# Kernel tuning notes

Hardware: AMD Instinct MI355X
Metric: run time of the kernel (lower is better)

Reference implementation:

```python
import jax, jax.numpy as jnp
import numpy as np

DIM = 1024
N_HEADS = 16
HEAD_DIM = DIM // N_HEADS


def setup_inputs() -> dict:
    key = jax.random.key(0)
    ks = jax.random.split(key, 5)
    scale = 1.0 / np.sqrt(DIM)
    x = jax.random.normal(ks[0], (2, 2048, DIM), dtype=jnp.float32)
    W_qkv = jax.random.normal(ks[1], (DIM, 3 * DIM), dtype=jnp.float32) * scale
    b_qkv = jax.random.normal(ks[2], (3 * DIM,), dtype=jnp.float32) * 0.01
    W_proj = jax.random.normal(ks[3], (DIM, DIM), dtype=jnp.float32) * scale
    b_proj = jax.random.normal(ks[4], (DIM,), dtype=jnp.float32) * 0.01
    return {"x": x, "W_qkv": W_qkv, "b_qkv": b_qkv, "W_proj": W_proj, "b_proj": b_proj}


def reference(x, W_qkv, b_qkv, W_proj, b_proj):
    B, T, C = x.shape
    qkv = x @ W_qkv + b_qkv  # [B,T,3C]
    q, k, v = jnp.split(qkv, 3, axis=2)
    # [B,T,C] -> [B,H,T,Dh]
    def heads(y):
        return y.reshape(B, T, N_HEADS, HEAD_DIM).transpose(0, 2, 1, 3)
    q, k, v = heads(q), heads(k), heads(v)
    inv_sqrt_dh = 1.0 / jnp.sqrt(jnp.asarray(HEAD_DIM, dtype=x.dtype))
    attn = jnp.einsum('bhqd,bhkd->bhqk', q, k) * inv_sqrt_dh
    attn = jax.nn.softmax(attn, axis=-1)
    out = jnp.einsum('bhqk,bhkd->bhqd', attn, v)
    out = out.transpose(0, 2, 1, 3).reshape(B, T, C)
    return out @ W_proj + b_proj
```

## Files before the change

kernel.cpp:

```cpp
#include <hip/hip_runtime.h>
#include <hip/hip_bf16.h>
#include <math.h>

using bf16 = __hip_bfloat16;

typedef __bf16 bf16x8 __attribute__((ext_vector_type(8)));
typedef __bf16 bf16x4 __attribute__((ext_vector_type(4)));
typedef float  f32x4  __attribute__((ext_vector_type(4)));
typedef float  f32x16 __attribute__((ext_vector_type(16)));

constexpr int Bb = 2;
constexpr int Ts = 2048;
constexpr int Cc = 1024;
constexpr int Hh = 16;
constexpr int Dh = 64;
constexpr int Mm = Bb * Ts;
constexpr int Nqkv = 3 * Cc;
constexpr int BHTD = Bb * Hh * Ts * Dh;

__device__ __forceinline__
void gll16(const __bf16* g, __bf16* l)
{
    __builtin_amdgcn_global_load_lds(
        (const __attribute__((address_space(1))) unsigned int*)g,
        (__attribute__((address_space(3))) unsigned int*)l,
        16, 0, 0);
}

__global__ __launch_bounds__(256)
void prep_all(const float* __restrict__ x, __bf16* __restrict__ Xb,
              const float* __restrict__ Wq, __bf16* __restrict__ Wqt,
              const float* __restrict__ Wp, __bf16* __restrict__ Wpt)
{
    __shared__ __bf16 tl[64][72];
    const int bid = blockIdx.x;
    const int t = threadIdx.x;

    if (bid < 4096) {
        int i = (bid * 256 + t) * 4;
        float4 v = *(const float4*)(x + i);
        bf16x4 o = { (__bf16)v.x, (__bf16)v.y, (__bf16)v.z, (__bf16)v.w };
        *(bf16x4*)(Xb + i) = o;
        return;
    }
    const float* W; __bf16* Wt; int cols, bx, by;
    if (bid < 4096 + 768) {
        W = Wq; Wt = Wqt; cols = Nqkv;
        bx = (bid - 4096) % 48; by = (bid - 4096) / 48;
    } else {
        W = Wp; Wt = Wpt; cols = Cc;
        bx = (bid - 4864) % 16; by = (bid - 4864) / 16;
    }
    const int c0 = bx * 64;
    const int r0 = by * 64;
    #pragma unroll
    for (int i = 0; i < 4; i++) {
        int e = t + 256 * i;
        int r = e >> 4, c4 = (e & 15) * 4;
        float4 v = *(const float4*)(W + (r0 + r) * cols + c0 + c4);
        bf16x4 o = { (__bf16)v.x, (__bf16)v.y, (__bf16)v.z, (__bf16)v.w };
        *(bf16x4*)&tl[r][c4] = o;
    }
    __syncthreads();
    #pragma unroll
    for (int i = 0; i < 4; i++) {
        int e = t + 256 * i;
        int n = e >> 4, k4 = (e & 15) * 4;
        bf16x4 o = { tl[k4][n], tl[k4 + 1][n], tl[k4 + 2][n], tl[k4 + 3][n] };
        *(bf16x4*)(Wt + (c0 + n) * 1024 + r0 + k4) = o;
    }
}

template<int BM>
__device__ __forceinline__
void gemm_core_tb(__bf16* sbuf,
                  const __bf16* __restrict__ A, const __bf16* __restrict__ Bt,
                  int m0, int n0, int wm, int wn, int quad, int l16, int t,
                  f32x4 (&acc)[4][4])
{
    constexpr int MT   = BM / 32;
    constexpr int AG   = BM / 64;
    constexpr int STEP = (BM + 128) * 32;

    const int wave = t >> 6;
    const int lane = t & 63;
    const int srow = lane >> 2;
    const int scol = ((lane & 3) ^ (srow & 3)) * 8;

    const __bf16* Ag = A  + (size_t)(m0 + wave * (BM / 4) + srow) * 1024 + scol;
    const __bf16* Bg = Bt + (size_t)(n0 + wave * 32 + srow) * 1024 + scol;

    {
        __bf16* Alp = sbuf;
        __bf16* Blp = sbuf + BM * 32;
        #pragma unroll
        for (int g = 0; g < AG; g++)
            gll16(Ag + (size_t)g * 16 * 1024, &Alp[(wave * (BM / 4) + g * 16) * 32]);
        gll16(Bg,                      &Blp[(wave * 32) * 32]);
        gll16(Bg + (size_t)16 * 1024,  &Blp[(wave * 32 + 16) * 32]);
    }

    const int cb = (quad ^ (l16 & 3)) * 16;

    for (int j = 0; j < 32; j++) {
        const int p = j % 3;
        if (j < 31) {
            const int pn = (j + 1) % 3;
            const int k1 = (j + 1) * 32;
            __bf16* Alp = sbuf + pn * STEP;
            __bf16* Blp = Alp + BM * 32;
            #pragma unroll
            for (int g = 0; g < AG; g++)
                gll16(Ag + k1 + (size_t)g * 16 * 1024,
                      &Alp[(wave * (BM / 4) + g * 16) * 32]);
            gll16(Bg + k1,                     &Blp[(wave * 32) * 32]);
            gll16(Bg + k1 + (size_t)16 * 1024, &Blp[(wave * 32 + 16) * 32]);
            if constexpr (AG == 2) asm volatile("s_waitcnt vmcnt(4)" ::: "memory");
            else                   asm volatile("s_waitcnt vmcnt(3)" ::: "memory");
        } else {
            asm volatile("s_waitcnt vmcnt(0)" ::: "memory");
        }
        __builtin_amdgcn_s_barrier();
        __builtin_amdgcn_sched_barrier(0);

        const char* Alp = (const char*)(sbuf + p * STEP);
        const char* Blp = (const char*)(sbuf + p * STEP + BM * 32);
        bf16x8 af[MT], bfr[4];
        #pragma unroll
        for (int mt = 0; mt < MT; mt++)
            af[mt] = *(const bf16x8*)(Alp + (wm * (BM / 2) + mt * 16 + l16) * 64 + cb);
        #pragma unroll
        for (int nt = 0; nt < 4; nt++)
            bfr[nt] = *(const bf16x8*)(Blp + (wn * 64 + nt * 16 + l16) * 64 + cb);
        #pragma unroll
        for (int mt = 0; mt < MT; mt++)
            #pragma unroll
            for (int nt = 0; nt < 4; nt++)
                acc[mt][nt] = __builtin_amdgcn_mfma_f32_16x16x32_bf16(
                    af[mt], bfr[nt], acc[mt][nt], 0, 0, 0);
    }
    __syncthreads();
}

__global__ __launch_bounds__(512, 2)
void qkv_mfma(const __bf16* __restrict__ A, const __bf16* __restrict__ Bt,
              const float* __restrict__ bias, __bf16* __restrict__ qkv)
{
    __shared__ __align__(16) __bf16 smem[2 * 512 * 64];
    typedef __bf16 (*ebuf_p)[64][72];
    ebuf_p ebuf = (ebuf_p)smem;

    const int t    = threadIdx.x;
    const int wave = t >> 6;
    const int lane = t & 63;
    const int quad = lane >> 4;
    const int l16  = lane & 15;
    const int wm   = wave >> 2;
    const int wn   = wave & 3;
    const int bid  = blockIdx.x;
    const int swb  = (bid & 7) * 24 + (bid >> 3);
    const int n0 = (swb % 12) * 256;
    const int m0 = (swb / 12) * 256;

    f32x4 acc[8][4];
    #pragma unroll
    for (int i = 0; i < 8; i++)
        #pragma unroll
        for (int j = 0; j < 4; j++)
            acc[i][j] = f32x4{0.f, 0.f, 0.f, 0.f};

    const int srow = lane >> 3;
    const int scol = ((lane & 7) ^ srow) * 8;
    const __bf16* Ag = A  + (size_t)(m0 + wave * 32 + srow) * 1024 + scol;
    const __bf16* Bg = Bt + (size_t)(n0 + wave * 32 + srow) * 1024 + scol;

    {
        __bf16* Alp = smem;
        __bf16* Blp = smem + 256 * 64;
        #pragma unroll
        for (int g = 0; g < 4; g++) {
            gll16(Ag + (size_t)g * 8 * 1024, &Alp[(wave * 32 + g * 8) * 64]);
            gll16(Bg + (size_t)g * 8 * 1024, &Blp[(wave * 32 + g * 8) * 64]);
        }
    }

    for (int j = 0; j < 16; j++) {
        const int p = j & 1;
        asm volatile("s_waitcnt vmcnt(0)" ::: "memory");
        __builtin_amdgcn_s_barrier();
        __builtin_amdgcn_sched_barrier(0);
        if (j < 15) {
            const int k1 = (j + 1) * 64;
            __bf16* Alp = smem + (p ^ 1) * (512 * 64);
            __bf16* Blp = Alp + 256 * 64;
            #pragma unroll
            for (int g = 0; g < 4; g++) {
                gll16(Ag + k1 + (size_t)g * 8 * 1024, &Alp[(wave * 32 + g * 8) * 64]);
                gll16(Bg + k1 + (size_t)g * 8 * 1024, &Blp[(wave * 32 + g * 8) * 64]);
            }
        }
        const char* Alp = (const char*)(smem + p * (512 * 64));
        const char* Blp = Alp + 256 * 64 * 2;

        #pragma unroll
        for (int kk = 0; kk < 2; kk++) {
            const int cb = ((kk * 4 + quad) ^ (l16 & 7)) * 16;
            bf16x8 af[8], bfr[4];
            #pragma unroll
            for (int mt = 0; mt < 8; mt++)
                af[mt] = *(const bf16x8*)(Alp + (wm * 128 + mt * 16 + l16) * 128 + cb);
            #pragma unroll
            for (int nt = 0; nt < 4; nt++)
                bfr[nt] = *(const bf16x8*)(Blp + (wn * 64 + nt * 16 + l16) * 128 + cb);
            __builtin_amdgcn_s_setprio(1);
            #pragma unroll
            for (int mt = 0; mt < 8; mt++)
                #pragma unroll
                for (int nt = 0; nt < 4; nt++)
                    acc[mt][nt] = __builtin_amdgcn_mfma_f32_16x16x32_bf16(
                        af[mt], bfr[nt], acc[mt][nt], 0, 0, 0);
            __builtin_amdgcn_s_setprio(0);
        }
    }
    __syncthreads();

    const int nw0 = n0 + wn * 64;
    const int which = nw0 >> 10;
    const int h = (nw0 & 1023) >> 6;

    #pragma unroll
    for (int hh = 0; hh < 2; hh++) {
        if (which == 2) {
            #pragma unroll
            for (int nt = 0; nt < 4; nt++) {
                float bs = bias[nw0 + nt * 16 + l16];
                #pragma unroll
                for (int ml = 0; ml < 4; ml++) {
                    const int mt = hh * 4 + ml;
                    #pragma unroll
                    for (int r = 0; r < 4; r++)
                        ebuf[wave][nt * 16 + l16][ml * 16 + quad * 4 + r] =
                            (__bf16)(acc[mt][nt][r] + bs);
                }
            }
            const int mbase = m0 + wm * 128 + hh * 64;
            const int b   = mbase >> 11;
            const int tt0 = mbase & 2047;
            __bf16* vb0 = &qkv[2 * (size_t)BHTD +
                               ((size_t)(b * 16 + h) * 64) * 2048 + tt0];
            const int q4 = (lane & 3) * 16;
            #pragma unroll
            for (int p2 = 0; p2 < 4; p2++) {
                const int d = 16 * p2 + (lane >> 2);
                const __bf16* src = &ebuf[wave][d][q4];
                __bf16* drow = vb0 + (size_t)d * 2048 + q4;
                *(bf16x8*)drow       = *(const bf16x8*)src;
                *(bf16x8*)(drow + 8) = *(const bf16x8*)(src + 8);
            }
        } else {
            #pragma unroll
            for (int nt = 0; nt < 4; nt++) {
                float bs = bias[nw0 + nt * 16 + l16];
                #pragma unroll
                for (int ml = 0; ml < 4; ml++) {
                    const int mt = hh * 4 + ml;
                    #pragma unroll
                    for (int r = 0; r < 4; r++)
                        ebuf[wave][ml * 16 + quad * 4 + r][nt * 16 + l16] =
                            (__bf16)(acc[mt][nt][r] + bs);
                }
            }
            int m = m0 + wm * 128 + hh * 64 + lane;
            int b = m >> 11;
            int tt = m & 2047;
            __bf16* dst = &qkv[which * (size_t)BHTD +
                               (((size_t)(b * 16 + h) * 2048 + tt) * 64)];
            #pragma unroll
            for (int c = 0; c < 8; c++)
                *(bf16x8*)(dst + c * 8) = *(const bf16x8*)&ebuf[wave][lane][c * 8];
        }
    }
}

__global__ __launch_bounds__(256)
void proj_mfma(const __bf16* __restrict__ A, const __bf16* __restrict__ Bt,
               const float* __restrict__ bias, float* __restrict__ out)
{
    __shared__ __align__(16) __bf16 smem[3 * (64 + 128) * 32];

    const int t    = threadIdx.x;
    const int wave = t >> 6;
    const int lane = t & 63;
    const int quad = lane >> 4;
    const int l16  = lane & 15;
    const int wm   = wave >> 1, wn = wave & 1;
    const int bid  = blockIdx.x;
    const int n0 = (bid & 7) * 128;
    const int m0 = (bid >> 3) * 64;

    f32x4 acc[4][4];
    #pragma unroll
    for (int i = 0; i < 4; i++)
        #pragma unroll
        for (int j = 0; j < 4; j++)
            acc[i][j] = f32x4{0.f, 0.f, 0.f, 0.f};

    gemm_core_tb<64>(smem, A, Bt, m0, n0, wm, wn, quad, l16, t, acc);

    #pragma unroll
    for (int nt = 0; nt < 4; nt++) {
        int n = n0 + wn * 64 + nt * 16 + l16;
        float bs = bias[n];
        #pragma unroll
        for (int mt = 0; mt < 2; mt++) {
            #pragma unroll
            for (int r = 0; r < 4; r++) {
                int m = m0 + wm * 32 + mt * 16 + quad * 4 + r;
                out[m * 1024 + n] = acc[mt][nt][r] + bs;
            }
        }
    }
}

__global__ __launch_bounds__(512, 2)
void attn_mfma(const __bf16* __restrict__ Q, const __bf16* __restrict__ K,
               const __bf16* __restrict__ VT, __bf16* __restrict__ O)
{
    __shared__ __bf16 sK[2][3][64 * 64];
    __shared__ __bf16 sV[2][3][64 * 64];
    __shared__ float  slsum[4][2][64];

    const int t    = threadIdx.x;
    const int wave = t >> 6;
    const int lane = t & 63;
    const int qg   = wave & 3;
    const int kh   = wave >> 2;
    const int c    = lane & 31;
    const int hi   = lane >> 5;
    const int hx   = hi * 16;
    const int sw   = (c & 7) << 4;

    const int blk = blockIdx.x;
    const int bh  = blk & 31;
    const int qc  = blk >> 5;
    const int q0  = qc * 256 + qg * 64;

    const __bf16* Qp = Q  + ((size_t)bh * Ts + q0) * Dh;
    const __bf16* Kp = K  + (size_t)bh * Ts * Dh;
    const __bf16* Vp = VT + (size_t)bh * Dh * Ts;

    const float qscale = 0.125f * 1.44269504088896f;
    bf16x8 qf[2][4];
    #pragma unroll
    for (int qs = 0; qs < 2; qs++)
        #pragma unroll
        for (int ds = 0; ds < 4; ds++) {
            bf16x8 v = *(const bf16x8*)(Qp + (qs * 32 + c) * Dh + ds * 16 + hi * 8);
            #pragma unroll
            for (int i = 0; i < 8; i++) v[i] = (__bf16)(qscale * (float)v[i]);
            qf[qs][ds] = v;
        }

    f32x16 accO[2][2];
    #pragma unroll
    for (int qs = 0; qs < 2; qs++)
        #pragma unroll
        for (int dt = 0; dt < 2; dt++)
            #pragma unroll
            for (int i = 0; i < 16; i++) accO[qs][dt][i] = 0.f;
    float lsum[2] = {0.f, 0.f};

    const f32x16 z16 = {0.f, 0.f, 0.f, 0.f, 0.f, 0.f, 0.f, 0.f,
                        0.f, 0.f, 0.f, 0.f, 0.f, 0.f, 0.f, 0.f};

    const int r0 = qg * 8 + (lane >> 3);
    const int s8 = ((lane & 7) ^ (r0 & 7)) * 8;
    const __bf16* kg0 = Kp + (size_t)(kh * 1024 + r0) * Dh + s8;
    const __bf16* kg1 = kg0 + 32 * Dh;
    const __bf16* vg0 = Vp + (size_t)r0 * Ts + kh * 1024 + s8;
    const __bf16* vg1 = vg0 + (size_t)32 * Ts;

    gll16(kg0, &sK[kh][0][qg * 512]);
    gll16(kg1, &sK[kh][0][2048 + qg * 512]);
    gll16(vg0, &sV[kh][0][qg * 512]);
    gll16(vg1, &sV[kh][0][2048 + qg * 512]);

    for (int j = 0; j < 16; j++) {
        const int p = j % 3;
        if (j < 15) {
            const int pn = (j + 1) % 3;
            gll16(kg0 + (j + 1) * 4096, &sK[kh][pn][qg * 512]);
            gll16(kg1 + (j + 1) * 4096, &sK[kh][pn][2048 + qg * 512]);
            gll16(vg0 + (j + 1) * 64,   &sV[kh][pn][qg * 512]);
            gll16(vg1 + (j + 1) * 64,   &sV[kh][pn][2048 + qg * 512]);
            asm volatile("s_waitcnt vmcnt(4)" ::: "memory");
        } else {
            asm volatile("s_waitcnt vmcnt(0)" ::: "memory");
        }
        __builtin_amdgcn_s_barrier();
        __builtin_amdgcn_sched_barrier(0);

        const char* kb = (const char*)&sK[kh][p][0];
        const char* vb = (const char*)&sV[kh][p][0];

        bf16x8 kf[2][4];
        #pragma unroll
        for (int kt = 0; kt < 2; kt++) {
            const char* rbase = kb + (kt * 32 + c) * 128;
            #pragma unroll
            for (int ds = 0; ds < 4; ds++)
                kf[kt][ds] = *(const bf16x8*)(rbase + ((ds * 32 + hx) ^ sw));
        }

        f32x16 st[2][2];
        __builtin_amdgcn_s_setprio(1);
        #pragma unroll
        for (int kt = 0; kt < 2; kt++)
            #pragma unroll
            for (int qs = 0; qs < 2; qs++)
                st[qs][kt] = __builtin_amdgcn_mfma_f32_32x32x16_bf16(
                    kf[kt][0], qf[qs][0], z16, 0, 0, 0);
        #pragma unroll
        for (int ds = 1; ds < 4; ds++)
            #pragma unroll
            for (int kt = 0; kt < 2; kt++)
                #pragma unroll
                for (int qs = 0; qs < 2; qs++)
                    st[qs][kt] = __builtin_amdgcn_mfma_f32_32x32x16_bf16(
                        kf[kt][ds], qf[qs][ds], st[qs][kt], 0, 0, 0);
        __builtin_amdgcn_s_setprio(0);

        bf16x8 pa[2][4];
        #pragma unroll
        for (int qs = 0; qs < 2; qs++) {
            unsigned pk[2][8];
            #pragma unroll
            for (int kt = 0; kt < 2; kt++) {
                float sum0 = 0.f, sum1 = 0.f;
                #pragma unroll
                for (int r = 0; r < 16; r++) {
                    float pv = __builtin_amdgcn_exp2f(st[qs][kt][r]);
                    st[qs][kt][r] = pv;
                    if (r & 1) sum1 += pv; else sum0 += pv;
                }
                lsum[qs] += sum0 + sum1;
                #pragma unroll
                for (int r2 = 0; r2 < 8; r2++) {
                    unsigned d;
                    asm("v_cvt_pk_bf16_f32 %0, %1, %2"
                        : "=v"(d)
                        : "v"(st[qs][kt][2 * r2]), "v"(st[qs][kt][2 * r2 + 1]));
                    pk[kt][r2] = d;
                }
            }
            #pragma unroll
            for (int s = 0; s < 4; s++) {
                const int kt = s >> 1, r4 = (s & 1) * 4;
                unsigned x0 = pk[kt][r4 + 0], y0 = pk[kt][r4 + 2];
                unsigned x1 = pk[kt][r4 + 1], y1 = pk[kt][r4 + 3];
                asm("v_permlane32_swap_b32 %0, %1" : "+v"(x0), "+v"(y0));
                asm("v_permlane32_swap_b32 %0, %1" : "+v"(x1), "+v"(y1));
                union { unsigned u[4]; bf16x8 b; } pu;
                pu.u[0] = x0; pu.u[1] = x1; pu.u[2] = y0; pu.u[3] = y1;
                pa[qs][s] = pu.b;
            }
        }

        __builtin_amdgcn_s_setprio(1);
        #pragma unroll
        for (int s = 0; s < 4; s++)
            #pragma unroll
            for (int dt = 0; dt < 2; dt++) {
                bf16x8 vf = *(const bf16x8*)(vb + (dt * 32 + c) * 128 +
                                             ((s * 32 + hx) ^ sw));
                #pragma unroll
                for (int qs = 0; qs < 2; qs++)
                    accO[qs][dt] = __builtin_amdgcn_mfma_f32_32x32x16_bf16(
                        pa[qs][s], vf, accO[qs][dt], 0, 0, 0);
            }
        __builtin_amdgcn_s_setprio(0);
    }

    __syncthreads();

    float* pb = (qg < 2) ? (float*)&sK[0][0][0] + qg * 4096
                         : (float*)&sV[0][0][0] + (qg - 2) * 4096;
    if (kh == 1) {
        #pragma unroll
        for (int qs = 0; qs < 2; qs++) {
            #pragma unroll
            for (int dt = 0; dt < 2; dt++)
                #pragma unroll
                for (int r = 0; r < 16; r++)
                    pb[((qs * 2 + dt) << 10) + (r << 6) + lane] = accO[qs][dt][r];
            slsum[qg][qs][lane] = lsum[qs];
        }
    }
    __syncthreads();
    if (kh == 0) {
        #pragma unroll
        for (int qs = 0; qs < 2; qs++) {
            #pragma unroll
            for (int dt = 0; dt < 2; dt++)
                #pragma unroll
                for (int r = 0; r < 16; r++)
                    accO[qs][dt][r] += pb[((qs * 2 + dt) << 10) + (r << 6) + lane];
            lsum[qs] += slsum[qg][qs][lane];
        }

        const int b = bh >> 4, h = bh & 15;
        #pragma unroll
        for (int qs = 0; qs < 2; qs++) {
            float l = lsum[qs] + __shfl_xor(lsum[qs], 32);
            float linv = 1.f / l;
            #pragma unroll
            for (int r = 0; r < 16; r++) {
                const int qrow = (r & 3) + 8 * (r >> 2) + 4 * hi;
                float inv = __shfl(linv, qrow);
                __bf16* Op = O + ((size_t)(b * Ts + q0 + qs * 32 + qrow)) * Cc +
                             h * 64 + c;
                Op[0]  = (__bf16)(accO[qs][0][r] * inv);
                Op[32] = (__bf16)(accO[qs][1][r] * inv);
            }
        }
    }
}

extern "C" void kernel_launch(void* const* d_in, const int* in_sizes, int n_in,
                              void* d_out, int out_size, void* d_ws, size_t ws_size,
                              hipStream_t stream)
{
    (void)in_sizes; (void)n_in; (void)out_size; (void)ws_size;
    const float* x     = (const float*)d_in[0];
    const float* Wqkv  = (const float*)d_in[1];
    const float* bqkv  = (const float*)d_in[2];
    const float* Wproj = (const float*)d_in[3];
    const float* bproj = (const float*)d_in[4];
    float* out = (float*)d_out;

    __bf16* ws   = (__bf16*)d_ws;
    __bf16* Qw   = ws;
    __bf16* XbAO = ws + 3 * (size_t)BHTD;
    __bf16* Wqt  = XbAO + (size_t)Mm * Cc;
    __bf16* Wpt  = Wqt + (size_t)Nqkv * Cc;

    prep_all<<<dim3(5120), 256, 0, stream>>>(x, XbAO, Wqkv, Wqt, Wproj, Wpt);
    qkv_mfma<<<dim3(192), 512, 0, stream>>>(XbAO, Wqt, bqkv, Qw);
    attn_mfma<<<dim3(256), 512, 0, stream>>>(
        Qw, Qw + BHTD, Qw + 2 * (size_t)BHTD, XbAO);
    proj_mfma<<<dim3(512), 256, 0, stream>>>(XbAO, Wpt, bproj, out);
}
```

Before: 177.8 us.

## Enlarge proj GEMM tile to 128x128 with BK=64 double buffering; coarsen x conversion

The projection GEMM moves from a 64x128 tile with a three-stage BK=32 pipeline to a 128x128 tile with double-buffered BK=64 loads, an 8-way XOR swizzle and MFMA priority hints. Its grid is halved to 256 blocks. The intent is more reuse per loaded tile and fewer barriers per unit of K. The x-to-bf16 conversion in prep_all now does four chunks per block, which cuts the block count and removes the now-unused shared gemm core. The costs are fewer blocks to fill the CUs in proj, which may underfill a 256-CU device, and a full vmcnt(0) wait each iteration that reduces load/compute overlap.

Result: no change. 177.2 us (-0.4%).

```diff
diff --git a/kernel.cpp b/kernel.cpp
--- a/kernel.cpp
+++ b/kernel.cpp
@@ -36,20 +36,23 @@
     const int bid = blockIdx.x;
     const int t = threadIdx.x;
 
-    if (bid < 4096) {
-        int i = (bid * 256 + t) * 4;
-        float4 v = *(const float4*)(x + i);
-        bf16x4 o = { (__bf16)v.x, (__bf16)v.y, (__bf16)v.z, (__bf16)v.w };
-        *(bf16x4*)(Xb + i) = o;
+    if (bid < 1024) {
+        #pragma unroll
+        for (int s = 0; s < 4; s++) {
+            int i = (bid * 256 + t + s * 262144) * 4;
+            float4 v = *(const float4*)(x + i);
+            bf16x4 o = { (__bf16)v.x, (__bf16)v.y, (__bf16)v.z, (__bf16)v.w };
+            *(bf16x4*)(Xb + i) = o;
+        }
         return;
     }
     const float* W; __bf16* Wt; int cols, bx, by;
-    if (bid < 4096 + 768) {
+    if (bid < 1024 + 768) {
         W = Wq; Wt = Wqt; cols = Nqkv;
-        bx = (bid - 4096) % 48; by = (bid - 4096) / 48;
+        bx = (bid - 1024) % 48; by = (bid - 1024) / 48;
     } else {
         W = Wp; Wt = Wpt; cols = Cc;
-        bx = (bid - 4864) % 16; by = (bid - 4864) / 16;
+        bx = (bid - 1792) % 16; by = (bid - 1792) / 16;
     }
     const int c0 = bx * 64;
     const int r0 = by * 64;
@@ -69,77 +72,6 @@
         bf16x4 o = { tl[k4][n], tl[k4 + 1][n], tl[k4 + 2][n], tl[k4 + 3][n] };
         *(bf16x4*)(Wt + (c0 + n) * 1024 + r0 + k4) = o;
     }
-}
-
-template<int BM>
-__device__ __forceinline__
-void gemm_core_tb(__bf16* sbuf,
-                  const __bf16* __restrict__ A, const __bf16* __restrict__ Bt,
-                  int m0, int n0, int wm, int wn, int quad, int l16, int t,
-                  f32x4 (&acc)[4][4])
-{
-    constexpr int MT   = BM / 32;
-    constexpr int AG   = BM / 64;
-    constexpr int STEP = (BM + 128) * 32;
-
-    const int wave = t >> 6;
-    const int lane = t & 63;
-    const int srow = lane >> 2;
-    const int scol = ((lane & 3) ^ (srow & 3)) * 8;
-
-    const __bf16* Ag = A  + (size_t)(m0 + wave * (BM / 4) + srow) * 1024 + scol;
-    const __bf16* Bg = Bt + (size_t)(n0 + wave * 32 + srow) * 1024 + scol;
-
-    {
-        __bf16* Alp = sbuf;
-        __bf16* Blp = sbuf + BM * 32;
-        #pragma unroll
-        for (int g = 0; g < AG; g++)
-            gll16(Ag + (size_t)g * 16 * 1024, &Alp[(wave * (BM / 4) + g * 16) * 32]);
-        gll16(Bg,                      &Blp[(wave * 32) * 32]);
-        gll16(Bg + (size_t)16 * 1024,  &Blp[(wave * 32 + 16) * 32]);
-    }
-
-    const int cb = (quad ^ (l16 & 3)) * 16;
-
-    for (int j = 0; j < 32; j++) {
-        const int p = j % 3;
-        if (j < 31) {
-            const int pn = (j + 1) % 3;
-            const int k1 = (j + 1) * 32;
-            __bf16* Alp = sbuf + pn * STEP;
-            __bf16* Blp = Alp + BM * 32;
-            #pragma unroll
-            for (int g = 0; g < AG; g++)
-                gll16(Ag + k1 + (size_t)g * 16 * 1024,
-                      &Alp[(wave * (BM / 4) + g * 16) * 32]);
-            gll16(Bg + k1,                     &Blp[(wave * 32) * 32]);
-            gll16(Bg + k1 + (size_t)16 * 1024, &Blp[(wave * 32 + 16) * 32]);
-            if constexpr (AG == 2) asm volatile("s_waitcnt vmcnt(4)" ::: "memory");
-            else                   asm volatile("s_waitcnt vmcnt(3)" ::: "memory");
-        } else {
-            asm volatile("s_waitcnt vmcnt(0)" ::: "memory");
-        }
-        __builtin_amdgcn_s_barrier();
-        __builtin_amdgcn_sched_barrier(0);
-
-        const char* Alp = (const char*)(sbuf + p * STEP);
-        const char* Blp = (const char*)(sbuf + p * STEP + BM * 32);
-        bf16x8 af[MT], bfr[4];
-        #pragma unroll
-        for (int mt = 0; mt < MT; mt++)
-            af[mt] = *(const bf16x8*)(Alp + (wm * (BM / 2) + mt * 16 + l16) * 64 + cb);
-        #pragma unroll
-        for (int nt = 0; nt < 4; nt++)
-            bfr[nt] = *(const bf16x8*)(Blp + (wn * 64 + nt * 16 + l16) * 64 + cb);
-        #pragma unroll
-        for (int mt = 0; mt < MT; mt++)
-            #pragma unroll
-            for (int nt = 0; nt < 4; nt++)
-                acc[mt][nt] = __builtin_amdgcn_mfma_f32_16x16x32_bf16(
-                    af[mt], bfr[nt], acc[mt][nt], 0, 0, 0);
-    }
-    __syncthreads();
 }
 
 __global__ __launch_bounds__(512, 2)
@@ -286,7 +218,7 @@
 void proj_mfma(const __bf16* __restrict__ A, const __bf16* __restrict__ Bt,
                const float* __restrict__ bias, float* __restrict__ out)
 {
-    __shared__ __align__(16) __bf16 smem[3 * (64 + 128) * 32];
+    __shared__ __align__(16) __bf16 smem[2 * 256 * 64];
 
     const int t    = threadIdx.x;
     const int wave = t >> 6;
@@ -296,7 +228,7 @@
     const int wm   = wave >> 1, wn = wave & 1;
     const int bid  = blockIdx.x;
     const int n0 = (bid & 7) * 128;
-    const int m0 = (bid >> 3) * 64;
+    const int m0 = (bid >> 3) * 128;
 
     f32x4 acc[4][4];
     #pragma unroll
@@ -305,17 +237,69 @@
         for (int j = 0; j < 4; j++)
             acc[i][j] = f32x4{0.f, 0.f, 0.f, 0.f};
 
-    gemm_core_tb<64>(smem, A, Bt, m0, n0, wm, wn, quad, l16, t, acc);
+    const int srow = lane >> 3;
+    const int scol = ((lane & 7) ^ srow) * 8;
+    const __bf16* Ag = A  + (size_t)(m0 + wave * 32 + srow) * 1024 + scol;
+    const __bf16* Bg = Bt + (size_t)(n0 + wave * 32 + srow) * 1024 + scol;
+
+    {
+        __bf16* Alp = smem;
+        __bf16* Blp = smem + 128 * 64;
+        #pragma unroll
+        for (int g = 0; g < 4; g++) {
+            gll16(Ag + (size_t)g * 8 * 1024, &Alp[(wave * 32 + g * 8) * 64]);
+            gll16(Bg + (size_t)g * 8 * 1024, &Blp[(wave * 32 + g * 8) * 64]);
+        }
+    }
+
+    for (int j = 0; j < 16; j++) {
+        const int p = j & 1;
+        asm volatile("s_waitcnt vmcnt(0)" ::: "memory");
+        __builtin_amdgcn_s_barrier();
+        __builtin_amdgcn_sched_barrier(0);
+        if (j < 15) {
+            const int k1 = (j + 1) * 64;
+            __bf16* Alp = smem + (p ^ 1) * (256 * 64);
+            __bf16* Blp = Alp + 128 * 64;
+            #pragma unroll
+            for (int g = 0; g < 4; g++) {
+                gll16(Ag + k1 + (size_t)g * 8 * 1024, &Alp[(wave * 32 + g * 8) * 64]);
+                gll16(Bg + k1 + (size_t)g * 8 * 1024, &Blp[(wave * 32 + g * 8) * 64]);
+            }
+        }
+        const char* Alp = (const char*)(smem + p * (256 * 64));
+        const char* Blp = Alp + 128 * 64 * 2;
+
+        #pragma unroll
+        for (int kk = 0; kk < 2; kk++) {
+            const int cb = ((kk * 4 + quad) ^ (l16 & 7)) * 16;
+            bf16x8 af[4], bfr[4];
+            #pragma unroll
+            for (int mt = 0; mt < 4; mt++)
+                af[mt] = *(const bf16x8*)(Alp + (wm * 64 + mt * 16 + l16) * 128 + cb);
+            #pragma unroll
+            for (int nt = 0; nt < 4; nt++)
+                bfr[nt] = *(const bf16x8*)(Blp + (wn * 64 + nt * 16 + l16) * 128 + cb);
+            __builtin_amdgcn_s_setprio(1);
+            #pragma unroll
+            for (int mt = 0; mt < 4; mt++)
+                #pragma unroll
+                for (int nt = 0; nt < 4; nt++)
+                    acc[mt][nt] = __builtin_amdgcn_mfma_f32_16x16x32_bf16(
+                        af[mt], bfr[nt], acc[mt][nt], 0, 0, 0);
+            __builtin_amdgcn_s_setprio(0);
+        }
+    }
 
     #pragma unroll
     for (int nt = 0; nt < 4; nt++) {
         int n = n0 + wn * 64 + nt * 16 + l16;
         float bs = bias[n];
         #pragma unroll
-        for (int mt = 0; mt < 2; mt++) {
+        for (int mt = 0; mt < 4; mt++) {
             #pragma unroll
             for (int r = 0; r < 4; r++) {
-                int m = m0 + wm * 32 + mt * 16 + quad * 4 + r;
+                int m = m0 + wm * 64 + mt * 16 + quad * 4 + r;
                 out[m * 1024 + n] = acc[mt][nt][r] + bs;
             }
         }
@@ -544,9 +528,9 @@
     __bf16* Wqt  = XbAO + (size_t)Mm * Cc;
     __bf16* Wpt  = Wqt + (size_t)Nqkv * Cc;
 
-    prep_all<<<dim3(5120), 256, 0, stream>>>(x, XbAO, Wqkv, Wqt, Wproj, Wpt);
+    prep_all<<<dim3(2048), 256, 0, stream>>>(x, XbAO, Wqkv, Wqt, Wproj, Wpt);
     qkv_mfma<<<dim3(192), 512, 0, stream>>>(XbAO, Wqt, bqkv, Qw);
     attn_mfma<<<dim3(256), 512, 0, stream>>>(
         Qw, Qw + BHTD, Qw + 2 * (size_t)BHTD, XbAO);
-    proj_mfma<<<dim3(512), 256, 0, stream>>>(XbAO, Wpt, bproj, out);
+    proj_mfma<<<dim3(256), 256, 0, stream>>>(XbAO, Wpt, bproj, out);
 }
```
